# Performance work log

Measured on AMD Instinct MI355X. Metric: run time of the kernel, lower is better.

The kernel has to match this reference:

```python
import jax, jax.numpy as jnp
import numpy as np

B, S, D, H = 2, 2048, 1024, 16
DK = D // H


def setup_inputs() -> dict:
    key = jax.random.key(0)
    ks = jax.random.split(key, 12)
    scale = 1.0 / np.sqrt(D)
    inp = {
        "pre_Q": jax.random.normal(ks[0], (B, S, D), jnp.float32),
        "pre_K": jax.random.normal(ks[1], (B, S, D), jnp.float32),
        "pre_V": jax.random.normal(ks[2], (B, S, D), jnp.float32),
        "Wq": jax.random.normal(ks[3], (D, D), jnp.float32) * scale,
        "bq": jnp.zeros((D,), jnp.float32),
        "Wk": jax.random.normal(ks[4], (D, D), jnp.float32) * scale,
        "bk": jnp.zeros((D,), jnp.float32),
        "Wv": jax.random.normal(ks[5], (D, D), jnp.float32) * scale,
        "bv": jnp.zeros((D,), jnp.float32),
        "Wo": jax.random.normal(ks[6], (D, D), jnp.float32) * scale,
        "bo": jnp.zeros((D,), jnp.float32),
        "mask": jnp.ones((B, 1, 1, S), jnp.int32),
    }
    return inp


def _split_heads(x):
    # (B, S, D) -> (B, H, S, DK)
    return x.reshape(B, S, H, DK).transpose(0, 2, 1, 3)


def reference(pre_Q, pre_K, pre_V, Wq, bq, Wk, bk, Wv, bv, Wo, bo, mask):
    # linear projections (torch nn.Linear: x @ W.T + b)
    Q = _split_heads(pre_Q @ Wq.T + bq)
    K = _split_heads(pre_K @ Wk.T + bk)
    V = _split_heads(pre_V @ Wv.T + bv)
    # scaled dot-product attention; dropout is identity in eval mode
    scores = jnp.einsum("bhqd,bhkd->bhqk", Q, K) / np.sqrt(DK).astype(np.float32)
    scores = jnp.where(mask == 0, jnp.float32(-1e9), scores)
    weights = jax.nn.softmax(scores, axis=-1)
    ctx = jnp.einsum("bhqk,bhkd->bhqd", weights, V)  # (B, H, S, DK)
    concat = ctx.transpose(0, 2, 1, 3).reshape(B, S, D)
    return concat @ Wo.T + bo
```

## Files before the change

kernel.cpp:

```cpp
#include <hip/hip_runtime.h>

#define SS 2048
#define DD 1024
#define HH 16
#define MM 4096
#define KK 1024

typedef __attribute__((ext_vector_type(8))) short bf16x8;
typedef __attribute__((ext_vector_type(4))) float f32x4;
typedef __attribute__((ext_vector_type(16))) float f32x16;
typedef __attribute__((ext_vector_type(4))) float float4_t;
typedef __attribute__((ext_vector_type(4))) short short4_t;

__device__ __forceinline__ short f2bf(float f) {
    union { float f; unsigned u; } x; x.f = f;
    unsigned r = x.u + 0x7fffu + ((x.u >> 16) & 1u);
    return (short)(r >> 16);
}

__device__ __forceinline__ f32x4 mfma16(bf16x8 a, bf16x8 b, f32x4 c) {
    return __builtin_amdgcn_mfma_f32_16x16x32_bf16(a, b, c, 0, 0, 0);
}
__device__ __forceinline__ f32x16 mfma32(bf16x8 a, bf16x8 b, f32x16 c) {
    return __builtin_amdgcn_mfma_f32_32x32x16_bf16(a, b, c, 0, 0, 0);
}

__device__ __forceinline__ void gl_lds16(const void* g, void* l) {
    __builtin_amdgcn_global_load_lds(
        (const __attribute__((address_space(1))) void*)g,
        (__attribute__((address_space(3))) void*)l, 16, 0, 0);
}

__device__ __forceinline__ float exp2a(float x) {
    float r; asm("v_exp_f32 %0, %1" : "=v"(r) : "v"(x)); return r;
}
__device__ __forceinline__ int cvtpk(float lo, float hi) {
    int r; asm("v_cvt_pk_bf16_f32 %0, %1, %2" : "=v"(r) : "v"(lo), "v"(hi)); return r;
}
__device__ __forceinline__ void pswap(int& a, int& b) {
    asm("v_permlane32_swap_b32 %0, %1" : "+v"(a), "+v"(b));
}

__global__ __launch_bounds__(256)
void convX(const float* __restrict__ x0, const float* __restrict__ x1,
           const float* __restrict__ x2, short* __restrict__ dst) {
    const float* s = (blockIdx.y == 0) ? x0 : (blockIdx.y == 1) ? x1 : x2;
    const size_t i = ((size_t)blockIdx.x * 256 + threadIdx.x) * 8;
    float4_t a = *(const float4_t*)(s + i);
    float4_t b = *(const float4_t*)(s + i + 4);
    bf16x8 o;
#pragma unroll
    for (int e = 0; e < 4; ++e) { o[e] = f2bf(a[e]); o[4 + e] = f2bf(b[e]); }
    *(bf16x8*)(dst + (size_t)blockIdx.y * MM * KK + i) = o;
}

__global__ __launch_bounds__(256)
void convW(const float* __restrict__ w0, const float* __restrict__ w1,
           const float* __restrict__ w2, const float* __restrict__ w3,
           short* __restrict__ dst) {
    const float* s = (blockIdx.y == 0) ? w0 : (blockIdx.y == 1) ? w1
                   : (blockIdx.y == 2) ? w2 : w3;
    const size_t i = ((size_t)blockIdx.x * 256 + threadIdx.x) * 8;
    float4_t a = *(const float4_t*)(s + i);
    float4_t b = *(const float4_t*)(s + i + 4);
    bf16x8 o;
#pragma unroll
    for (int e = 0; e < 4; ++e) { o[e] = f2bf(a[e]); o[4 + e] = f2bf(b[e]); }
    *(bf16x8*)(dst + (size_t)blockIdx.y * KK * KK + i) = o;
}

__device__ __forceinline__ void gemm_loop(const short* __restrict__ A,
                                          const short* __restrict__ Bw,
                                          int m0, int n0,
                                          short* As, short* Bs,
                                          f32x4 acc[4][4]) {
    const int tid = threadIdx.x;
    const int lane = tid & 63, w = tid >> 6;
    const int wr = w >> 1, wc = w & 1;
    const int lr = lane & 15, lg = lane >> 4;

    const int c1 = tid + 256;
    const int r0 = tid >> 2, o0 = (tid & 3) * 8;
    const int r1 = c1 >> 2, o1 = (c1 & 3) * 8;
    const short* ga0 = A + (size_t)(m0 + r0) * KK + o0;
    const short* ga1 = A + (size_t)(m0 + r1) * KK + o1;
    const short* gb0 = Bw + (size_t)(n0 + r0) * KK + o0;
    const short* gb1 = Bw + (size_t)(n0 + r1) * KK + o1;
    char* lA = (char*)As + tid * 16;
    char* lB = (char*)Bs + tid * 16;

#define GSTAGE(buf, kofs)                                  \
    { gl_lds16(ga0 + (kofs), lA + (buf) * 8192);           \
      gl_lds16(ga1 + (kofs), lA + 4096 + (buf) * 8192);    \
      gl_lds16(gb0 + (kofs), lB + (buf) * 8192);           \
      gl_lds16(gb1 + (kofs), lB + 4096 + (buf) * 8192); }

    GSTAGE(0, 0);
    __syncthreads();
    int cur = 0;
    for (int kt = 0; kt < KK / 32; ++kt) {
        if (kt + 1 < KK / 32) GSTAGE(cur ^ 1, (kt + 1) * 32);
        const char* ba = (const char*)As + cur * 8192;
        const char* bb = (const char*)Bs + cur * 8192;
        bf16x8 af[4], bfr[4];
#pragma unroll
        for (int i = 0; i < 4; ++i) {
            af[i]  = *(const bf16x8*)(ba + (wr * 64 + i * 16 + lr) * 64 + lg * 16);
            bfr[i] = *(const bf16x8*)(bb + (wc * 64 + i * 16 + lr) * 64 + lg * 16);
        }
#pragma unroll
        for (int mi = 0; mi < 4; ++mi)
#pragma unroll
            for (int ni = 0; ni < 4; ++ni)
                acc[mi][ni] = mfma16(af[mi], bfr[ni], acc[mi][ni]);
        __syncthreads();
        cur ^= 1;
    }
#undef GSTAGE
}

__global__ __launch_bounds__(256, 2)
void qkv_gemm(const short* __restrict__ Xb, const short* __restrict__ Wb,
              const float* __restrict__ bq, const float* __restrict__ bk,
              const float* __restrict__ bv,
              short* __restrict__ Qo, short* __restrict__ Ko, short* __restrict__ Vto) {
    __shared__ __align__(16) short As[2 * 4096];
    __shared__ __align__(16) short Bs[2 * 4096];
    const int z = blockIdx.z;
    const short* A = Xb + (size_t)z * MM * KK;
    const short* W = Wb + (size_t)z * KK * KK;
    const float* bias = (z == 0) ? bq : (z == 1) ? bk : bv;
    const float scale = (z == 0) ? 0.125f * 1.44269504088896f : 1.0f;
    const int m0 = blockIdx.x * 128, n0 = blockIdx.y * 128;

    f32x4 zero = {0.f, 0.f, 0.f, 0.f};
    f32x4 acc[4][4];
#pragma unroll
    for (int i = 0; i < 4; ++i)
#pragma unroll
        for (int j = 0; j < 4; ++j) acc[i][j] = zero;

    gemm_loop(A, W, m0, n0, As, Bs, acc);

    const int tid = threadIdx.x;
    const int lane = tid & 63, w = tid >> 6;
    const int wr = w >> 1, wc = w & 1;
    const int lr = lane & 15, lg = lane >> 4;

#pragma unroll
    for (int mi = 0; mi < 4; ++mi) {
        const int mbase = m0 + wr * 64 + mi * 16 + lg * 4;
        const int b = mbase >> 11, s = mbase & 2047;
#pragma unroll
        for (int ni = 0; ni < 4; ++ni) {
            const int n = n0 + wc * 64 + ni * 16 + lr;
            const float bvv = bias[n];
            const int h = n >> 6, dk = n & 63;
            if (z == 2) {
                short4_t pk;
#pragma unroll
                for (int r = 0; r < 4; ++r) pk[r] = f2bf(acc[mi][ni][r] + bvv);
                *(short4_t*)(Vto + ((size_t)((b * HH + h) * 64 + dk) << 11) + s) = pk;
            } else {
                short* dst = (z == 0) ? Qo : Ko;
#pragma unroll
                for (int r = 0; r < 4; ++r)
                    dst[((size_t)((b * HH + h) * SS + (s + r)) << 6) + dk] =
                        f2bf((acc[mi][ni][r] + bvv) * scale);
            }
        }
    }
}

__global__ __launch_bounds__(256, 2)
void out_gemm(const short* __restrict__ ctx, const short* __restrict__ Wo,
              const float* __restrict__ bo, float* __restrict__ out) {
    __shared__ __align__(16) short As[2 * 4096];
    __shared__ __align__(16) short Bs[2 * 4096];
    const int m0 = blockIdx.x * 128, n0 = blockIdx.y * 128;

    f32x4 zero = {0.f, 0.f, 0.f, 0.f};
    f32x4 acc[4][4];
#pragma unroll
    for (int i = 0; i < 4; ++i)
#pragma unroll
        for (int j = 0; j < 4; ++j) acc[i][j] = zero;

    gemm_loop(ctx, Wo, m0, n0, As, Bs, acc);

    const int tid = threadIdx.x;
    const int lane = tid & 63, w = tid >> 6;
    const int wr = w >> 1, wc = w & 1;
    const int lr = lane & 15, lg = lane >> 4;

#pragma unroll
    for (int mi = 0; mi < 4; ++mi)
#pragma unroll
        for (int ni = 0; ni < 4; ++ni) {
            const int n = n0 + wc * 64 + ni * 16 + lr;
            const float bvv = bo[n];
#pragma unroll
            for (int r = 0; r < 4; ++r) {
                const int m = m0 + wr * 64 + mi * 16 + lg * 4 + r;
                out[(size_t)m * KK + n] = acc[mi][ni][r] + bvv;
            }
        }
}

__global__ __launch_bounds__(256, 2)
void attn_kernel(const short* __restrict__ Qg, const short* __restrict__ Kg,
                 const short* __restrict__ Vtg, const int* __restrict__ mask,
                 short* __restrict__ ctxb) {
    __shared__ __align__(16) short Ks[2][4096];
    __shared__ __align__(16) short Vs[2][4096];

    const int tid = threadIdx.x, w = tid >> 6, lane = tid & 63;
    const int l31 = lane & 31, hi = lane >> 5;
    const int bh = blockIdx.y, b = bh >> 4, h = bh & 15;
    const int q0w = blockIdx.x * 128 + w * 32;

    const short* Qh = Qg + (size_t)bh * SS * 64;
    const short* Kh = Kg + (size_t)bh * SS * 64;
    const short* Vh = Vtg + (size_t)bh * 64 * SS;
    const int* mrow = mask + b * SS;

    bf16x8 qf[4];
#pragma unroll
    for (int t = 0; t < 4; ++t)
        qf[t] = *(const bf16x8*)(Qh + (q0w + l31) * 64 + t * 16 + hi * 8);

    f32x16 octx0, octx1;
#pragma unroll
    for (int r = 0; r < 16; ++r) { octx0[r] = 0.f; octx1[r] = 0.f; }
    float mrun = -1e30f, lrun = 0.f;

    const int tq = (tid >> 6) & 3;
    const short* gk0 = Kh + (l31) * 64 + tq * 16 + hi * 8;
    const short* gk1 = Kh + (32 + l31) * 64 + tq * 16 + hi * 8;
    const short* gv0 = Vh + (size_t)(l31) * SS + tq * 16 + hi * 8;
    const short* gv1 = Vh + (size_t)(32 + l31) * SS + tq * 16 + hi * 8;
    char* lK = (char*)Ks + tid * 16;
    char* lV = (char*)Vs + tid * 16;

#define ASTAGE(buf, key0)                                      \
    { gl_lds16(gk0 + (key0) * 64, lK + (buf) * 8192);          \
      gl_lds16(gk1 + (key0) * 64, lK + 4096 + (buf) * 8192);   \
      gl_lds16(gv0 + (key0), lV + (buf) * 8192);               \
      gl_lds16(gv1 + (key0), lV + 4096 + (buf) * 8192); }

    ASTAGE(0, 0);
    __syncthreads();
    int cur = 0;

    for (int it = 0; it < SS / 64; ++it) {
        const int key0 = it * 64;
        if (it + 1 < SS / 64) ASTAGE(cur ^ 1, key0 + 64);

        const char* cK = (const char*)Ks + cur * 8192;
        const char* cV = (const char*)Vs + cur * 8192;

        f32x16 s0, s1;
#pragma unroll
        for (int r = 0; r < 16; ++r) { s0[r] = 0.f; s1[r] = 0.f; }
#pragma unroll
        for (int t = 0; t < 4; ++t) {
            bf16x8 a0 = *(const bf16x8*)(cK + ((0 * 4 + t) * 64 + lane) * 16);
            bf16x8 a1 = *(const bf16x8*)(cK + ((1 * 4 + t) * 64 + lane) * 16);
            s0 = mfma32(a0, qf[t], s0);
            s1 = mfma32(a1, qf[t], s1);
        }

        const int mk = mrow[key0 + lane];
        if (!__all(mk != 0)) {
#pragma unroll
            for (int r = 0; r < 16; ++r) {
                const int kl = (r & 3) + 8 * (r >> 2) + 4 * hi;
                if (mrow[key0 + kl] == 0) s0[r] = -1e9f;
                if (mrow[key0 + 32 + kl] == 0) s1[r] = -1e9f;
            }
        }

        float tv[16];
#pragma unroll
        for (int r = 0; r < 16; ++r) tv[r] = fmaxf(s0[r], s1[r]);
#pragma unroll
        for (int off = 8; off >= 1; off >>= 1)
#pragma unroll
            for (int r = 0; r < 8; ++r)
                if (r < off) tv[r] = fmaxf(tv[r], tv[r + off]);
        float tm = tv[0];
        tm = fmaxf(tm, __shfl_xor(tm, 32));

        if (!__all(tm <= mrun + 8.0f)) {
            const float mnew = fmaxf(mrun, tm);
            const float alpha = exp2a(mrun - mnew);
            lrun *= alpha;
#pragma unroll
            for (int r = 0; r < 16; ++r) {
                const int ql = (r & 3) + 8 * (r >> 2) + 4 * hi;
                const float aq = __shfl(alpha, ql);
                octx0[r] *= aq;
                octx1[r] *= aq;
            }
            mrun = mnew;
        }

#pragma unroll
        for (int r = 0; r < 16; ++r) {
            s0[r] = exp2a(s0[r] - mrun);
            s1[r] = exp2a(s1[r] - mrun);
        }
        float sv[16];
#pragma unroll
        for (int r = 0; r < 16; ++r) sv[r] = s0[r] + s1[r];
#pragma unroll
        for (int off = 8; off >= 1; off >>= 1)
#pragma unroll
            for (int r = 0; r < 8; ++r)
                if (r < off) sv[r] += sv[r + off];
        float rs = sv[0];
        rs += __shfl_xor(rs, 32);
        lrun += rs;

        bf16x8 pa[4];
#pragma unroll
        for (int kb = 0; kb < 2; ++kb) {
            const f32x16& sv16 = kb ? s1 : s0;
#pragma unroll
            for (int half = 0; half < 2; ++half) {
                const int base = half * 8;
                int A  = cvtpk(sv16[base + 0], sv16[base + 1]);
                int Bw = cvtpk(sv16[base + 2], sv16[base + 3]);
                int Cw = cvtpk(sv16[base + 4], sv16[base + 5]);
                int Dw = cvtpk(sv16[base + 6], sv16[base + 7]);
                pswap(A, Cw);
                pswap(Bw, Dw);
                union { int wv[4]; bf16x8 v; } u;
                u.wv[0] = A; u.wv[1] = Bw; u.wv[2] = Cw; u.wv[3] = Dw;
                pa[kb * 2 + half] = u.v;
            }
        }

#pragma unroll
        for (int kk = 0; kk < 4; ++kk) {
            bf16x8 v0 = *(const bf16x8*)(cV + ((0 * 4 + kk) * 64 + lane) * 16);
            bf16x8 v1 = *(const bf16x8*)(cV + ((1 * 4 + kk) * 64 + lane) * 16);
            octx0 = mfma32(pa[kk], v0, octx0);
            octx1 = mfma32(pa[kk], v1, octx1);
        }

        __syncthreads();
        cur ^= 1;
    }
#undef ASTAGE

    const float linv = 1.f / lrun;
#pragma unroll
    for (int r = 0; r < 16; ++r) {
        const int ql = (r & 3) + 8 * (r >> 2) + 4 * hi;
        const float li = __shfl(linv, ql);
        short* orow = ctxb + (size_t)(b * SS + q0w + ql) * DD + h * 64 + l31;
        orow[0]  = f2bf(octx0[r] * li);
        orow[32] = f2bf(octx1[r] * li);
    }
}

extern "C" void kernel_launch(void* const* d_in, const int* in_sizes, int n_in,
                              void* d_out, int out_size, void* d_ws, size_t ws_size,
                              hipStream_t stream) {
    const float* preQ = (const float*)d_in[0];
    const float* preK = (const float*)d_in[1];
    const float* preV = (const float*)d_in[2];
    const float* Wq   = (const float*)d_in[3];
    const float* bq   = (const float*)d_in[4];
    const float* Wk   = (const float*)d_in[5];
    const float* bk   = (const float*)d_in[6];
    const float* Wv   = (const float*)d_in[7];
    const float* bv   = (const float*)d_in[8];
    const float* Wo   = (const float*)d_in[9];
    const float* bo   = (const float*)d_in[10];
    const int*   mask = (const int*)d_in[11];
    float* out = (float*)d_out;

    char* ws = (char*)d_ws;
    short* Xb  = (short*)(ws);
    short* Wb  = (short*)(ws + (size_t)25165824);
    short* Qw  = (short*)(ws + (size_t)33554432);
    short* Kw  = (short*)(ws + (size_t)41943040);
    short* Vtw = (short*)(ws + (size_t)50331648);
    short* Ctx = (short*)(ws + (size_t)58720256);

    convX<<<dim3(2048, 3), 256, 0, stream>>>(preQ, preK, preV, Xb);
    convW<<<dim3(512, 4), 256, 0, stream>>>(Wq, Wk, Wv, Wo, Wb);
    qkv_gemm<<<dim3(32, 8, 3), 256, 0, stream>>>(Xb, Wb, bq, bk, bv, Qw, Kw, Vtw);
    attn_kernel<<<dim3(16, 32), 256, 0, stream>>>(Qw, Kw, Vtw, mask, Ctx);
    out_gemm<<<dim3(32, 8), 256, 0, stream>>>(Ctx, Wb + (size_t)3 * KK * KK, bo, out);
}
```

Measured before the change: 240.5 us.

## Split attention over key halves with combine kernel; deepen GEMM K-tile to 64

The attention kernel now splits the key range into two halves along a new grid dimension, doubling the block count from 512 to 1024. Each half writes unnormalized bf16 partial outputs plus its running max and sum, and a new combine kernel merges them with exp2 rescaling. The goal is to fill more CUs and raise occupancy, since launch bounds go to 4 blocks per CU. Separately, the shared GEMM loop loads 64-wide K tiles, halving the number of barriers per K, at the cost of doubled LDS and an extra kernel pass over the partial outputs.

```diff
diff --git a/kernel.cpp b/kernel.cpp
--- a/kernel.cpp
+++ b/kernel.cpp
@@ -16,6 +16,10 @@
     union { float f; unsigned u; } x; x.f = f;
     unsigned r = x.u + 0x7fffu + ((x.u >> 16) & 1u);
     return (short)(r >> 16);
+}
+__device__ __forceinline__ float bf2f(short s) {
+    union { unsigned u; float f; } x; x.u = ((unsigned)(unsigned short)s) << 16;
+    return x.f;
 }
 
 __device__ __forceinline__ f32x4 mfma16(bf16x8 a, bf16x8 b, f32x4 c) {
@@ -79,40 +83,40 @@
     const int wr = w >> 1, wc = w & 1;
     const int lr = lane & 15, lg = lane >> 4;
 
-    const int c1 = tid + 256;
-    const int r0 = tid >> 2, o0 = (tid & 3) * 8;
-    const int r1 = c1 >> 2, o1 = (c1 & 3) * 8;
-    const short* ga0 = A + (size_t)(m0 + r0) * KK + o0;
-    const short* ga1 = A + (size_t)(m0 + r1) * KK + o1;
-    const short* gb0 = Bw + (size_t)(n0 + r0) * KK + o0;
-    const short* gb1 = Bw + (size_t)(n0 + r1) * KK + o1;
+    const int r0 = tid >> 3, o0 = (tid & 7) * 8;
+    const short* ga = A + (size_t)(m0 + r0) * KK + o0;
+    const short* gb = Bw + (size_t)(n0 + r0) * KK + o0;
     char* lA = (char*)As + tid * 16;
     char* lB = (char*)Bs + tid * 16;
 
-#define GSTAGE(buf, kofs)                                  \
-    { gl_lds16(ga0 + (kofs), lA + (buf) * 8192);           \
-      gl_lds16(ga1 + (kofs), lA + 4096 + (buf) * 8192);    \
-      gl_lds16(gb0 + (kofs), lB + (buf) * 8192);           \
-      gl_lds16(gb1 + (kofs), lB + 4096 + (buf) * 8192); }
+#define GSTAGE(buf, kofs)                                                     \
+    { _Pragma("unroll")                                                       \
+      for (int j = 0; j < 4; ++j) {                                           \
+          gl_lds16(ga + (size_t)j * 32 * KK + (kofs), lA + (buf) * 16384 + j * 4096); \
+          gl_lds16(gb + (size_t)j * 32 * KK + (kofs), lB + (buf) * 16384 + j * 4096); \
+      } }
 
     GSTAGE(0, 0);
     __syncthreads();
     int cur = 0;
-    for (int kt = 0; kt < KK / 32; ++kt) {
-        if (kt + 1 < KK / 32) GSTAGE(cur ^ 1, (kt + 1) * 32);
-        const char* ba = (const char*)As + cur * 8192;
-        const char* bb = (const char*)Bs + cur * 8192;
-        bf16x8 af[4], bfr[4];
-#pragma unroll
-        for (int i = 0; i < 4; ++i) {
-            af[i]  = *(const bf16x8*)(ba + (wr * 64 + i * 16 + lr) * 64 + lg * 16);
-            bfr[i] = *(const bf16x8*)(bb + (wc * 64 + i * 16 + lr) * 64 + lg * 16);
-        }
-#pragma unroll
-        for (int mi = 0; mi < 4; ++mi)
-#pragma unroll
-            for (int ni = 0; ni < 4; ++ni)
-                acc[mi][ni] = mfma16(af[mi], bfr[ni], acc[mi][ni]);
+    for (int kt = 0; kt < KK / 64; ++kt) {
+        if (kt + 1 < KK / 64) GSTAGE(cur ^ 1, (kt + 1) * 64);
+        const char* ba = (const char*)As + cur * 16384;
+        const char* bb = (const char*)Bs + cur * 16384;
+#pragma unroll
+        for (int ks = 0; ks < 2; ++ks) {
+            bf16x8 af[4], bfr[4];
+#pragma unroll
+            for (int i = 0; i < 4; ++i) {
+                af[i]  = *(const bf16x8*)(ba + (wr * 64 + i * 16 + lr) * 128 + ks * 64 + lg * 16);
+                bfr[i] = *(const bf16x8*)(bb + (wc * 64 + i * 16 + lr) * 128 + ks * 64 + lg * 16);
+            }
+#pragma unroll
+            for (int mi = 0; mi < 4; ++mi)
+#pragma unroll
+                for (int ni = 0; ni < 4; ++ni)
+                    acc[mi][ni] = mfma16(af[mi], bfr[ni], acc[mi][ni]);
+        }
         __syncthreads();
         cur ^= 1;
     }
@@ -124,8 +128,8 @@
               const float* __restrict__ bq, const float* __restrict__ bk,
               const float* __restrict__ bv,
               short* __restrict__ Qo, short* __restrict__ Ko, short* __restrict__ Vto) {
-    __shared__ __align__(16) short As[2 * 4096];
-    __shared__ __align__(16) short Bs[2 * 4096];
+    __shared__ __align__(16) short As[2 * 8192];
+    __shared__ __align__(16) short Bs[2 * 8192];
     const int z = blockIdx.z;
     const short* A = Xb + (size_t)z * MM * KK;
     const short* W = Wb + (size_t)z * KK * KK;
@@ -175,8 +179,8 @@
 __global__ __launch_bounds__(256, 2)
 void out_gemm(const short* __restrict__ ctx, const short* __restrict__ Wo,
               const float* __restrict__ bo, float* __restrict__ out) {
-    __shared__ __align__(16) short As[2 * 4096];
-    __shared__ __align__(16) short Bs[2 * 4096];
+    __shared__ __align__(16) short As[2 * 8192];
+    __shared__ __align__(16) short Bs[2 * 8192];
     const int m0 = blockIdx.x * 128, n0 = blockIdx.y * 128;
 
     f32x4 zero = {0.f, 0.f, 0.f, 0.f};
@@ -207,16 +211,17 @@
         }
 }
 
-__global__ __launch_bounds__(256, 2)
+__global__ __launch_bounds__(256, 4)
 void attn_kernel(const short* __restrict__ Qg, const short* __restrict__ Kg,
                  const short* __restrict__ Vtg, const int* __restrict__ mask,
-                 short* __restrict__ ctxb) {
+                 short* __restrict__ Po, float* __restrict__ Pm, float* __restrict__ Pl) {
     __shared__ __align__(16) short Ks[2][4096];
     __shared__ __align__(16) short Vs[2][4096];
 
     const int tid = threadIdx.x, w = tid >> 6, lane = tid & 63;
     const int l31 = lane & 31, hi = lane >> 5;
-    const int bh = blockIdx.y, b = bh >> 4, h = bh & 15;
+    const int bh = blockIdx.y, b = bh >> 4;
+    const int half = blockIdx.z;
     const int q0w = blockIdx.x * 128 + w * 32;
 
     const short* Qh = Qg + (size_t)bh * SS * 64;
@@ -248,13 +253,14 @@
       gl_lds16(gv0 + (key0), lV + (buf) * 8192);               \
       gl_lds16(gv1 + (key0), lV + 4096 + (buf) * 8192); }
 
-    ASTAGE(0, 0);
+    const int it0 = half * (SS / 128), it1 = it0 + (SS / 128);
+    ASTAGE(0, it0 * 64);
     __syncthreads();
     int cur = 0;
 
-    for (int it = 0; it < SS / 64; ++it) {
+    for (int it = it0; it < it1; ++it) {
         const int key0 = it * 64;
-        if (it + 1 < SS / 64) ASTAGE(cur ^ 1, key0 + 64);
+        if (it + 1 < it1) ASTAGE(cur ^ 1, key0 + 64);
 
         const char* cK = (const char*)Ks + cur * 8192;
         const char* cV = (const char*)Vs + cur * 8192;
@@ -327,8 +333,8 @@
         for (int kb = 0; kb < 2; ++kb) {
             const f32x16& sv16 = kb ? s1 : s0;
 #pragma unroll
-            for (int half = 0; half < 2; ++half) {
-                const int base = half * 8;
+            for (int halfp = 0; halfp < 2; ++halfp) {
+                const int base = halfp * 8;
                 int A  = cvtpk(sv16[base + 0], sv16[base + 1]);
                 int Bw = cvtpk(sv16[base + 2], sv16[base + 3]);
                 int Cw = cvtpk(sv16[base + 4], sv16[base + 5]);
@@ -337,7 +343,7 @@
                 pswap(Bw, Dw);
                 union { int wv[4]; bf16x8 v; } u;
                 u.wv[0] = A; u.wv[1] = Bw; u.wv[2] = Cw; u.wv[3] = Dw;
-                pa[kb * 2 + half] = u.v;
+                pa[kb * 2 + halfp] = u.v;
             }
         }
 
@@ -354,15 +360,44 @@
     }
 #undef ASTAGE
 
-    const float linv = 1.f / lrun;
+    const size_t pbase = (size_t)(half * 32 + bh) * SS;
 #pragma unroll
     for (int r = 0; r < 16; ++r) {
         const int ql = (r & 3) + 8 * (r >> 2) + 4 * hi;
-        const float li = __shfl(linv, ql);
-        short* orow = ctxb + (size_t)(b * SS + q0w + ql) * DD + h * 64 + l31;
-        orow[0]  = f2bf(octx0[r] * li);
-        orow[32] = f2bf(octx1[r] * li);
+        short* prow = Po + (pbase + q0w + ql) * 64 + l31;
+        prow[0]  = f2bf(octx0[r]);
+        prow[32] = f2bf(octx1[r]);
     }
+    if (hi == 0) {
+        Pm[pbase + q0w + l31] = mrun;
+        Pl[pbase + q0w + l31] = lrun;
+    }
+}
+
+__global__ __launch_bounds__(256)
+void attn_combine(const short* __restrict__ Po, const float* __restrict__ Pm,
+                  const float* __restrict__ Pl, short* __restrict__ ctxb) {
+    const int idx = blockIdx.x * 256 + threadIdx.x;
+    const int d0 = (idx & 7) * 8;
+    const int s  = (idx >> 3) & (SS - 1);
+    const int bh = idx >> 14;
+    const int b = bh >> 4, h = bh & 15;
+
+    const size_t i1 = (size_t)bh * SS + s;
+    const size_t i2 = (size_t)(32 + bh) * SS + s;
+    const float m1 = Pm[i1], m2 = Pm[i2];
+    const float l1 = Pl[i1], l2 = Pl[i2];
+    const float m = fmaxf(m1, m2);
+    const float w1 = exp2a(m1 - m), w2 = exp2a(m2 - m);
+    const float inv = 1.f / (l1 * w1 + l2 * w2);
+
+    bf16x8 o1 = *(const bf16x8*)(Po + i1 * 64 + d0);
+    bf16x8 o2 = *(const bf16x8*)(Po + i2 * 64 + d0);
+    bf16x8 o;
+#pragma unroll
+    for (int j = 0; j < 8; ++j)
+        o[j] = f2bf((bf2f(o1[j]) * w1 + bf2f(o2[j]) * w2) * inv);
+    *(bf16x8*)(ctxb + ((size_t)(b * SS + s)) * DD + h * 64 + d0) = o;
 }
 
 extern "C" void kernel_launch(void* const* d_in, const int* in_sizes, int n_in,
@@ -389,10 +424,14 @@
     short* Kw  = (short*)(ws + (size_t)41943040);
     short* Vtw = (short*)(ws + (size_t)50331648);
     short* Ctx = (short*)(ws + (size_t)58720256);
+    short* Po  = (short*)(ws + (size_t)67108864);
+    float* Pm  = (float*)(ws + (size_t)83886080);
+    float* Pl  = (float*)(ws + (size_t)84410368);
 
     convX<<<dim3(2048, 3), 256, 0, stream>>>(preQ, preK, preV, Xb);
     convW<<<dim3(512, 4), 256, 0, stream>>>(Wq, Wk, Wv, Wo, Wb);
     qkv_gemm<<<dim3(32, 8, 3), 256, 0, stream>>>(Xb, Wb, bq, bk, bv, Qw, Kw, Vtw);
-    attn_kernel<<<dim3(16, 32), 256, 0, stream>>>(Qw, Kw, Vtw, mask, Ctx);
+    attn_kernel<<<dim3(16, 32, 2), 256, 0, stream>>>(Qw, Kw, Vtw, mask, Po, Pm, Pl);
+    attn_combine<<<dim3(2048), 256, 0, stream>>>(Po, Pm, Pl, Ctx);
     out_gemm<<<dim3(32, 8), 256, 0, stream>>>(Ctx, Wb + (size_t)3 * KK * KK, bo, out);
 }
```

After: 263.4 us. 1.1x slower.
